# Kernel optimization log

Measured on AMD Instinct MI355X. Metric: run time of the kernel, lower is better.

The kernel has to match this reference:

```python
import jax, jax.numpy as jnp
import numpy as np

N = 100000   # nodes
R = 4        # relations
E = 200000   # edges per relation
IN = 256
HID = 64
OUT = 64
H = 8        # heads
NEG_SLOPE = 0.2


def setup_inputs() -> dict:
    key = jax.random.key(0)
    ks = jax.random.split(key, 13)
    s = 0.05
    return {
        "x": jax.random.normal(ks[0], (N, IN), jnp.float32),
        "src": jax.random.randint(ks[1], (R, E), 0, N),
        "dst": jax.random.randint(ks[2], (R, E), 0, N),
        "W0": jax.random.normal(ks[3], (R, IN, H * HID), jnp.float32) * s,
        "al0": jax.random.normal(ks[4], (R, H, HID), jnp.float32) * s,
        "ar0": jax.random.normal(ks[5], (R, H, HID), jnp.float32) * s,
        "W1": jax.random.normal(ks[6], (R, H * HID, H * HID), jnp.float32) * s,
        "al1": jax.random.normal(ks[7], (R, H, HID), jnp.float32) * s,
        "ar1": jax.random.normal(ks[8], (R, H, HID), jnp.float32) * s,
        "W2": jax.random.normal(ks[9], (R, H * HID, H * OUT), jnp.float32) * s,
        "al2": jax.random.normal(ks[10], (R, H, OUT), jnp.float32) * s,
        "ar2": jax.random.normal(ks[11], (R, H, OUT), jnp.float32) * s,
    }


def gat_layer(h, src, dst, W, al, ar):
    """Multi-relation GATConv layer; HeteroGraphConv sums ELU'd per-relation outputs.
    h: [N, in]; W: [R, in, H*O]; al/ar: [R, H, O]. Returns [N, H, O]."""
    n = h.shape[0]
    nheads, odim = al.shape[1], al.shape[2]
    acc = jnp.zeros((n, nheads, odim), h.dtype)
    for r in range(W.shape[0]):  # small fixed relation count
        f = (h @ W[r]).reshape(n, nheads, odim)          # [N,H,O]
        el = jnp.sum(f * al[r], axis=-1)                  # [N,H]
        er = jnp.sum(f * ar[r], axis=-1)                  # [N,H]
        s_r, d_r = src[r], dst[r]
        e = jax.nn.leaky_relu(el[s_r] + er[d_r], NEG_SLOPE)  # [E,H]
        # segment softmax over incoming edges per destination node
        m = jax.ops.segment_max(e, d_r, num_segments=n)
        m = jnp.where(jnp.isfinite(m), m, 0.0)
        ex = jnp.exp(e - m[d_r])
        denom = jax.ops.segment_sum(ex, d_r, num_segments=n)
        alpha = ex / (denom[d_r] + 1e-9)                  # [E,H]
        msg = f[s_r] * alpha[:, :, None]                  # [E,H,O]
        out_r = jax.ops.segment_sum(msg, d_r, num_segments=n)  # [N,H,O]
        acc = acc + jax.nn.elu(out_r)
    return acc


def reference(x, src, dst, W0, al0, ar0, W1, al1, ar1, W2, al2, ar2):
    h = gat_layer(x, src, dst, W0, al0, ar0).reshape(N, -1)   # flatten heads
    h = gat_layer(h, src, dst, W1, al1, ar1).reshape(N, -1)   # flatten heads
    h = gat_layer(h, src, dst, W2, al2, ar2).mean(axis=1)     # mean over heads
    return h
```

## Files before the change

kernel.cpp:

```cpp
#include <hip/hip_runtime.h>
#include <hip/hip_bf16.h>
#include <math.h>

#define NNODES 100000
#define NREL 4
#define NEDGE 200000
#define NH 8
#define FDIM 512
#define NMB256 391

typedef float f4 __attribute__((ext_vector_type(4)));
typedef __bf16 bf16x8 __attribute__((ext_vector_type(8)));
typedef __bf16 bf16x4 __attribute__((ext_vector_type(4)));

__device__ __forceinline__ float eluf(float v) { return v > 0.f ? v : expm1f(v); }
__device__ __forceinline__ void gload16(const __bf16* g, __bf16* l) {
  __builtin_amdgcn_global_load_lds((const __attribute__((address_space(1))) void*)g,
                                   (__attribute__((address_space(3))) void*)l, 16, 0, 0);
}

__global__ void k_conv(const float* __restrict__ in, __bf16* __restrict__ outp) {
  int i = (blockIdx.x * 256 + threadIdx.x) * 4;
  f4 v = *(const f4*)(in + i);
  bf16x4 o = {(__bf16)v.x, (__bf16)v.y, (__bf16)v.z, (__bf16)v.w};
  *(bf16x4*)(outp + i) = o;
}

__global__ void k_transW(const float* __restrict__ W, __bf16* __restrict__ Wt, int K) {
  __shared__ float tile[32][33];
  int r = blockIdx.z;
  const float* Wr = W + (size_t)r * K * FDIM;
  __bf16* Wtr = Wt + (size_t)r * FDIM * K;
  int k0 = blockIdx.x * 32, n0 = blockIdx.y * 32;
  int tx = threadIdx.x, ty = threadIdx.y;
  for (int i = ty; i < 32; i += 8)
    tile[i][tx] = Wr[(size_t)(k0 + i) * FDIM + n0 + tx];
  __syncthreads();
  for (int i = ty; i < 32; i += 8)
    Wtr[(size_t)(n0 + i) * K + k0 + tx] = (__bf16)tile[tx][i];
}

__global__ __launch_bounds__(512, 2) void k_gemm(const __bf16* __restrict__ A,
                                                 const __bf16* __restrict__ BT,
                                                 __bf16* __restrict__ C,
                                                 const float* __restrict__ al,
                                                 const float* __restrict__ ar,
                                                 __bf16* __restrict__ el,
                                                 __bf16* __restrict__ er, int M, int K) {
  __shared__ alignas(16) __bf16 lds[3][4][128 * 32];
  int t = threadIdx.x, l = t & 63, w = t >> 6;
  int nwg = gridDim.x, q8 = nwg >> 3, r8 = nwg & 7;
  int xx = blockIdx.x & 7, loc = blockIdx.x >> 3;
  int swz = (xx < r8 ? xx * (q8 + 1) : r8 * (q8 + 1) + (xx - r8) * q8) + loc;
  int m0 = (swz >> 1) * 256, n0 = (swz & 1) * 256;
  int wm = (w >> 2) * 128, wn = (w & 3) * 64;
  f4 acc[8][4] = {};

  int srow = t >> 2;
  int scol = ((t & 3) ^ (srow & 3)) * 8;
  const __bf16* pS[4];
  {
    int ra0 = m0 + srow;       if (ra0 >= M) ra0 = M - 1;
    int ra1 = m0 + 128 + srow; if (ra1 >= M) ra1 = M - 1;
    pS[0] = A + (size_t)ra0 * K + scol;
    pS[1] = A + (size_t)ra1 * K + scol;
    pS[2] = BT + (size_t)(n0 + srow) * K + scol;
    pS[3] = BT + (size_t)(n0 + 128 + srow) * K + scol;
  }
#define STG(tile, rgn) gload16(pS[rgn] + (size_t)(tile) * 32, &lds[(tile) % 3][rgn][t * 8])

  int roff = ((l >> 4) ^ (l & 3)) * 8;
  int areg = w >> 2;
  int breg = 2 + ((w & 3) >> 1);
  int brow0 = (w & 1) * 64;

  int nt = K >> 5;
#pragma unroll
  for (int g = 0; g < 4; g++) STG(0, g);
#pragma unroll
  for (int g = 0; g < 4; g++) STG(1, g);
  asm volatile("s_waitcnt vmcnt(4)" :::);
  __builtin_amdgcn_s_barrier();
  __builtin_amdgcn_sched_barrier(0);

  for (int k = 0; k < nt; k++) {
    int bk = k % 3;
    bool stg = (k + 2) < nt;
    bf16x8 b[4], af[4];
#pragma unroll
    for (int j = 0; j < 4; j++)
      b[j] = *(const bf16x8*)(&lds[bk][breg][(brow0 + j * 16 + (l & 15)) * 32 + roff]);
#pragma unroll
    for (int i = 0; i < 4; i++)
      af[i] = *(const bf16x8*)(&lds[bk][areg][(i * 16 + (l & 15)) * 32 + roff]);
    if (stg) { STG(k + 2, 0); STG(k + 2, 1); }
    __builtin_amdgcn_s_barrier();
    asm volatile("s_waitcnt lgkmcnt(0)" ::: "memory");
    __builtin_amdgcn_sched_barrier(0);
    __builtin_amdgcn_s_setprio(1);
#pragma unroll
    for (int i = 0; i < 4; i++)
#pragma unroll
      for (int j = 0; j < 4; j++)
        acc[i][j] = __builtin_amdgcn_mfma_f32_16x16x32_bf16(af[i], b[j], acc[i][j], 0, 0, 0);
    __builtin_amdgcn_s_setprio(0);
    __builtin_amdgcn_s_barrier();
    __builtin_amdgcn_sched_barrier(0);
#pragma unroll
    for (int i = 0; i < 4; i++)
      af[i] = *(const bf16x8*)(&lds[bk][areg][(64 + i * 16 + (l & 15)) * 32 + roff]);
    if (stg) { STG(k + 2, 2); STG(k + 2, 3); }
    if (k + 2 < nt)      asm volatile("s_waitcnt vmcnt(4)" :::);
    else if (k + 1 < nt) asm volatile("s_waitcnt vmcnt(0)" :::);
    __builtin_amdgcn_s_barrier();
    asm volatile("s_waitcnt lgkmcnt(0)" ::: "memory");
    __builtin_amdgcn_sched_barrier(0);
    __builtin_amdgcn_s_setprio(1);
#pragma unroll
    for (int i = 0; i < 4; i++)
#pragma unroll
      for (int j = 0; j < 4; j++)
        acc[4 + i][j] = __builtin_amdgcn_mfma_f32_16x16x32_bf16(af[i], b[j], acc[4 + i][j], 0, 0, 0);
    __builtin_amdgcn_s_setprio(0);
    __builtin_amdgcn_s_barrier();
    __builtin_amdgcn_sched_barrier(0);
  }
#undef STG

  int cn = n0 + wn + (l & 15);
  int rbase = m0 + wm + (l >> 4) * 4;
#pragma unroll
  for (int i = 0; i < 8; i++)
#pragma unroll
    for (int q2 = 0; q2 < 4; q2++) {
      int row = rbase + i * 16 + q2;
      if (row < M) {
#pragma unroll
        for (int j = 0; j < 4; j++)
          C[(size_t)row * FDIM + cn + j * 16] = (__bf16)acc[i][j][q2];
      }
    }

  int h = (n0 + wn) >> 6;
  float av[4], bv[4];
#pragma unroll
  for (int j = 0; j < 4; j++) {
    av[j] = al[h * 64 + j * 16 + (l & 15)];
    bv[j] = ar[h * 64 + j * 16 + (l & 15)];
  }
#pragma unroll
  for (int i = 0; i < 8; i++)
#pragma unroll
    for (int q2 = 0; q2 < 4; q2++) {
      float se = acc[i][0][q2] * av[0] + acc[i][1][q2] * av[1] +
                 acc[i][2][q2] * av[2] + acc[i][3][q2] * av[3];
      float sr = acc[i][0][q2] * bv[0] + acc[i][1][q2] * bv[1] +
                 acc[i][2][q2] * bv[2] + acc[i][3][q2] * bv[3];
      se += __shfl_xor(se, 1); se += __shfl_xor(se, 2);
      se += __shfl_xor(se, 4); se += __shfl_xor(se, 8);
      sr += __shfl_xor(sr, 1); sr += __shfl_xor(sr, 2);
      sr += __shfl_xor(sr, 4); sr += __shfl_xor(sr, 8);
      if ((l & 15) == 0) {
        int row = rbase + i * 16 + q2;
        if (row < M) {
          el[row * NH + h] = (__bf16)se;
          er[row * NH + h] = (__bf16)sr;
        }
      }
    }
}

__global__ void k_count(const int* __restrict__ dst, int* __restrict__ deg) {
  int e = blockIdx.x * 256 + threadIdx.x;
  int r = blockIdx.y;
  if (e < NEDGE) {
    int d = dst[(size_t)r * NEDGE + e];
    if ((unsigned)d < (unsigned)NNODES) atomicAdd(&deg[r * NNODES + d], 1);
  }
}

__global__ __launch_bounds__(256) void k_scan_a(const int* __restrict__ in, int* __restrict__ out,
                                                int* __restrict__ bsum, int n) {
  __shared__ int wsums[4];
  int t = threadIdx.x, lane = t & 63, w = t >> 6;
  int base = blockIdx.x * 1024 + t * 4;
  int v0 = base + 0 < n ? in[base + 0] : 0;
  int v1 = base + 1 < n ? in[base + 1] : 0;
  int v2 = base + 2 < n ? in[base + 2] : 0;
  int v3 = base + 3 < n ? in[base + 3] : 0;
  int tot = v0 + v1 + v2 + v3;
  int sc = tot;
#pragma unroll
  for (int off = 1; off < 64; off <<= 1) {
    int u = __shfl_up(sc, off);
    if (lane >= off) sc += u;
  }
  if (lane == 63) wsums[w] = sc;
  __syncthreads();
  int add = 0;
#pragma unroll
  for (int i = 0; i < 4; i++)
    if (i < w) add += wsums[i];
  int excl = add + sc - tot;
  if (base + 0 < n) out[base + 0] = excl;
  if (base + 1 < n) out[base + 1] = excl + v0;
  if (base + 2 < n) out[base + 2] = excl + v0 + v1;
  if (base + 3 < n) out[base + 3] = excl + v0 + v1 + v2;
  if (t == 255) bsum[blockIdx.x] = add + sc;
}

__global__ __launch_bounds__(256) void k_scan_b(int* __restrict__ bsum, int nb) {
  __shared__ int wsums[4];
  int t = threadIdx.x, lane = t & 63, w = t >> 6;
  int i0 = t * 2, i1 = t * 2 + 1;
  int v0 = i0 < nb ? bsum[i0] : 0;
  int v1 = i1 < nb ? bsum[i1] : 0;
  int tot = v0 + v1, sc = tot;
#pragma unroll
  for (int off = 1; off < 64; off <<= 1) {
    int u = __shfl_up(sc, off);
    if (lane >= off) sc += u;
  }
  if (lane == 63) wsums[w] = sc;
  __syncthreads();
  int add = 0;
#pragma unroll
  for (int i = 0; i < 4; i++)
    if (i < w) add += wsums[i];
  int excl = add + sc - tot;
  if (i0 < nb) bsum[i0] = excl;
  if (i1 < nb) bsum[i1] = excl + v0;
}

__global__ void k_scan_c(int* __restrict__ out, const int* __restrict__ bsum, int n) {
  int i = blockIdx.x * 256 + threadIdx.x;
  if (i < n) out[i] += bsum[i >> 10];
}

__global__ void k_scatter(const int* __restrict__ src, const int* __restrict__ dst,
                          const int* __restrict__ ptrf, int* __restrict__ cur,
                          int* __restrict__ csrc) {
  int e = blockIdx.x * 256 + threadIdx.x;
  int r = blockIdx.y;
  if (e >= NEDGE) return;
  int d = dst[(size_t)r * NEDGE + e];
  if ((unsigned)d >= (unsigned)NNODES) return;
  int slot = ptrf[r * NNODES + d] + atomicAdd(&cur[r * NNODES + d], 1);
  if ((unsigned)slot < (unsigned)(NREL * NEDGE))
    csrc[slot] = src[(size_t)r * NEDGE + e];
}

__global__ void k_agg(const __bf16* __restrict__ f, const __bf16* __restrict__ el,
                      const __bf16* __restrict__ er, const int* __restrict__ ptrf,
                      const int* __restrict__ deg, const int* __restrict__ csrc,
                      __bf16* __restrict__ accG, int writeMode) {
  int t = threadIdx.x;
  int l = t & 63;
  int d = blockIdx.x * 4 + (t >> 6);
  int h = l >> 3;
  int cnt = deg[d];
  float res[8] = {0.f, 0.f, 0.f, 0.f, 0.f, 0.f, 0.f, 0.f};
  if (cnt > 0) {
    int start = ptrf[d];
    if (start < 0) start = 0;
    if (start > NREL * NEDGE) start = NREL * NEDGE;
    if (cnt > NREL * NEDGE - start) cnt = NREL * NEDGE - start;
    float erh = (float)er[d * NH + h];
    float a[8] = {0.f, 0.f, 0.f, 0.f, 0.f, 0.f, 0.f, 0.f};
    float den = 0.f;
    for (int j = 0; j < cnt; j++) {
      int s = csrc[start + j];
      if ((unsigned)s >= (unsigned)NNODES) s = 0;
      float e = (float)el[s * NH + h] + erh;
      e = (e > 0.f) ? e : 0.2f * e;
      float ex = __expf(e);
      den += ex;
      bf16x8 fv = *(const bf16x8*)(f + (size_t)s * FDIM + l * 8);
#pragma unroll
      for (int i = 0; i < 8; i++) a[i] += ex * (float)fv[i];
    }
    float inv = 1.f / (den + 1e-9f);
#pragma unroll
    for (int i = 0; i < 8; i++) res[i] = eluf(a[i] * inv);
  } else if (!writeMode) {
    return;
  }
  __bf16* ap = accG + (size_t)d * FDIM + l * 8;
  bf16x8 o;
  if (writeMode) {
#pragma unroll
    for (int i = 0; i < 8; i++) o[i] = (__bf16)res[i];
  } else {
    bf16x8 cv = *(bf16x8*)ap;
#pragma unroll
    for (int i = 0; i < 8; i++) o[i] = (__bf16)((float)cv[i] + res[i]);
  }
  *(bf16x8*)ap = o;
}

__global__ void k_mean(const __bf16* __restrict__ acc, float* __restrict__ out) {
  int t = blockIdx.x * 256 + threadIdx.x;
  int n = t >> 6, o = t & 63;
  const __bf16* ap = acc + (size_t)n * FDIM + o;
  float s = 0.f;
#pragma unroll
  for (int h = 0; h < 8; h++) s += (float)ap[h * 64];
  out[t] = s * 0.125f;
}

extern "C" void kernel_launch(void* const* d_in, const int* in_sizes, int n_in,
                              void* d_out, int out_size, void* d_ws, size_t ws_size,
                              hipStream_t stream) {
  const float* x = (const float*)d_in[0];
  const int* srcp = (const int*)d_in[1];
  const int* dstp = (const int*)d_in[2];
  const float* Wl[3]  = {(const float*)d_in[3], (const float*)d_in[6], (const float*)d_in[9]};
  const float* alp[3] = {(const float*)d_in[4], (const float*)d_in[7], (const float*)d_in[10]};
  const float* arl[3] = {(const float*)d_in[5], (const float*)d_in[8], (const float*)d_in[11]};
  float* out = (float*)d_out;
  (void)in_sizes; (void)n_in; (void)out_size;

  auto rup = [](size_t b) { return (b + 255) & ~(size_t)255; };
  size_t need = 3 * rup((size_t)NNODES * FDIM * 2) +
                2 * rup((size_t)NNODES * NH * 2) +
                rup((size_t)NREL * FDIM * FDIM * 2) +
                3 * rup((size_t)NREL * NNODES * 4) +
                rup((size_t)NREL * NEDGE * 4) + rup(4096);
  if (ws_size < need) return;

  char* ws = (char*)d_ws;
  size_t off = 0;
  auto alloc = [&](size_t bytes) -> void* { void* p = ws + off; off += rup(bytes); return p; };
  __bf16* bufA = (__bf16*)alloc((size_t)NNODES * FDIM * 2);
  __bf16* bufB = (__bf16*)alloc((size_t)NNODES * FDIM * 2);
  __bf16* fbuf = (__bf16*)alloc((size_t)NNODES * FDIM * 2);
  __bf16* el   = (__bf16*)alloc((size_t)NNODES * NH * 2);
  __bf16* er   = (__bf16*)alloc((size_t)NNODES * NH * 2);
  __bf16* Wt   = (__bf16*)alloc((size_t)NREL * FDIM * FDIM * 2);
  int* deg  = (int*)alloc((size_t)NREL * NNODES * 4);
  int* ptrf = (int*)alloc((size_t)NREL * NNODES * 4);
  int* cur  = (int*)alloc((size_t)NREL * NNODES * 4);
  int* csrc = (int*)alloc((size_t)NREL * NEDGE * 4);
  int* bsum = (int*)alloc(4096);

  hipMemsetAsync(deg, 0, (size_t)NREL * NNODES * 4, stream);
  hipMemsetAsync(cur, 0, (size_t)NREL * NNODES * 4, stream);
  k_count<<<dim3((NEDGE + 255) / 256, NREL), 256, 0, stream>>>(dstp, deg);
  int ntot = NREL * NNODES;
  int nb1 = (ntot + 1023) / 1024;
  k_scan_a<<<nb1, 256, 0, stream>>>(deg, ptrf, bsum, ntot);
  k_scan_b<<<1, 256, 0, stream>>>(bsum, nb1);
  k_scan_c<<<(ntot + 255) / 256, 256, 0, stream>>>(ptrf, bsum, ntot);
  k_scatter<<<dim3((NEDGE + 255) / 256, NREL), 256, 0, stream>>>(srcp, dstp, ptrf, cur, csrc);

  k_conv<<<(NNODES * 256) / 1024, 256, 0, stream>>>(x, bufA);

  __bf16* inb = bufA;
  __bf16* outb = bufB;
  int ngrid = NMB256 * 2;
  for (int L = 0; L < 3; L++) {
    int K = (L == 0) ? 256 : FDIM;
    k_transW<<<dim3(K / 32, 16, NREL), dim3(32, 8), 0, stream>>>(Wl[L], Wt, K);
    for (int r = 0; r < NREL; r++) {
      k_gemm<<<ngrid, 512, 0, stream>>>(inb, Wt + (size_t)r * FDIM * K, fbuf,
                                        alp[L] + (size_t)r * 512,
                                        arl[L] + (size_t)r * 512,
                                        el, er, NNODES, K);
      k_agg<<<NNODES / 4, 256, 0, stream>>>(fbuf, el, er, ptrf + (size_t)r * NNODES,
                                            deg + (size_t)r * NNODES, csrc, outb,
                                            r == 0 ? 1 : 0);
    }
    __bf16* tmp = inb; inb = outb; outb = tmp;
  }
  k_mean<<<(NNODES * 64) / 256, 256, 0, stream>>>(inb, out);
}
```

Measured before the change: 2.263 ms.

## Replace LDS-pipelined GEMM with direct-load tiles; unroll aggregation; fuse final mean

The 256x256 LDS-staged, triple-buffered GEMM is replaced with a simpler 128x128 tile kernel in which each wave loads MFMA operands straight from global memory, with no LDS and no barriers. The edge aggregation loop is unrolled by two with separate accumulators to raise memory-level parallelism. The last layer's aggregation now does the head mean and writes fp32 output directly, removing the separate mean kernel and the bf16 accumulator round trip. Workspace is trimmed by aliasing the scatter scratch onto the feature buffer. The GEMM gives up LDS data reuse, which can raise global and L2 traffic.

```diff
diff --git a/kernel.cpp b/kernel.cpp
--- a/kernel.cpp
+++ b/kernel.cpp
@@ -7,17 +7,13 @@
 #define NEDGE 200000
 #define NH 8
 #define FDIM 512
-#define NMB256 391
+#define NMB 782
 
 typedef float f4 __attribute__((ext_vector_type(4)));
 typedef __bf16 bf16x8 __attribute__((ext_vector_type(8)));
 typedef __bf16 bf16x4 __attribute__((ext_vector_type(4)));
 
 __device__ __forceinline__ float eluf(float v) { return v > 0.f ? v : expm1f(v); }
-__device__ __forceinline__ void gload16(const __bf16* g, __bf16* l) {
-  __builtin_amdgcn_global_load_lds((const __attribute__((address_space(1))) void*)g,
-                                   (__attribute__((address_space(3))) void*)l, 16, 0, 0);
-}
 
 __global__ void k_conv(const float* __restrict__ in, __bf16* __restrict__ outp) {
   int i = (blockIdx.x * 256 + threadIdx.x) * 4;
@@ -40,97 +36,50 @@
     Wtr[(size_t)(n0 + i) * K + k0 + tx] = (__bf16)tile[tx][i];
 }
 
-__global__ __launch_bounds__(512, 2) void k_gemm(const __bf16* __restrict__ A,
-                                                 const __bf16* __restrict__ BT,
-                                                 __bf16* __restrict__ C,
-                                                 const float* __restrict__ al,
-                                                 const float* __restrict__ ar,
-                                                 __bf16* __restrict__ el,
-                                                 __bf16* __restrict__ er, int M, int K) {
-  __shared__ alignas(16) __bf16 lds[3][4][128 * 32];
+__global__ __launch_bounds__(256) void k_gemm(const __bf16* __restrict__ A,
+                                              const __bf16* __restrict__ BT,
+                                              __bf16* __restrict__ C,
+                                              const float* __restrict__ al,
+                                              const float* __restrict__ ar,
+                                              __bf16* __restrict__ el,
+                                              __bf16* __restrict__ er, int M, int K) {
   int t = threadIdx.x, l = t & 63, w = t >> 6;
   int nwg = gridDim.x, q8 = nwg >> 3, r8 = nwg & 7;
   int xx = blockIdx.x & 7, loc = blockIdx.x >> 3;
   int swz = (xx < r8 ? xx * (q8 + 1) : r8 * (q8 + 1) + (xx - r8) * q8) + loc;
-  int m0 = (swz >> 1) * 256, n0 = (swz & 1) * 256;
-  int wm = (w >> 2) * 128, wn = (w & 3) * 64;
-  f4 acc[8][4] = {};
-
-  int srow = t >> 2;
-  int scol = ((t & 3) ^ (srow & 3)) * 8;
-  const __bf16* pS[4];
-  {
-    int ra0 = m0 + srow;       if (ra0 >= M) ra0 = M - 1;
-    int ra1 = m0 + 128 + srow; if (ra1 >= M) ra1 = M - 1;
-    pS[0] = A + (size_t)ra0 * K + scol;
-    pS[1] = A + (size_t)ra1 * K + scol;
-    pS[2] = BT + (size_t)(n0 + srow) * K + scol;
-    pS[3] = BT + (size_t)(n0 + 128 + srow) * K + scol;
-  }
-#define STG(tile, rgn) gload16(pS[rgn] + (size_t)(tile) * 32, &lds[(tile) % 3][rgn][t * 8])
-
-  int roff = ((l >> 4) ^ (l & 3)) * 8;
-  int areg = w >> 2;
-  int breg = 2 + ((w & 3) >> 1);
-  int brow0 = (w & 1) * 64;
+  int m0 = (swz >> 2) * 128, n0 = (swz & 3) * 128;
+  int wm = (w >> 1) * 64, wn = (w & 1) * 64;
+  f4 acc[4][4] = {};
+
+  const __bf16* pa[4];
+  const __bf16* pb[4];
+#pragma unroll
+  for (int i = 0; i < 4; i++) {
+    int row = m0 + wm + i * 16 + (l & 15);
+    if (row >= M) row = M - 1;
+    pa[i] = A + (size_t)row * K + (l >> 4) * 8;
+    pb[i] = BT + (size_t)(n0 + wn + i * 16 + (l & 15)) * K + (l >> 4) * 8;
+  }
 
   int nt = K >> 5;
-#pragma unroll
-  for (int g = 0; g < 4; g++) STG(0, g);
-#pragma unroll
-  for (int g = 0; g < 4; g++) STG(1, g);
-  asm volatile("s_waitcnt vmcnt(4)" :::);
-  __builtin_amdgcn_s_barrier();
-  __builtin_amdgcn_sched_barrier(0);
-
-  for (int k = 0; k < nt; k++) {
-    int bk = k % 3;
-    bool stg = (k + 2) < nt;
-    bf16x8 b[4], af[4];
-#pragma unroll
-    for (int j = 0; j < 4; j++)
-      b[j] = *(const bf16x8*)(&lds[bk][breg][(brow0 + j * 16 + (l & 15)) * 32 + roff]);
+#pragma unroll 2
+  for (int kt = 0; kt < nt; kt++) {
+    bf16x8 a[4], b[4];
+#pragma unroll
+    for (int i = 0; i < 4; i++) a[i] = *(const bf16x8*)(pa[i] + kt * 32);
+#pragma unroll
+    for (int j = 0; j < 4; j++) b[j] = *(const bf16x8*)(pb[j] + kt * 32);
 #pragma unroll
     for (int i = 0; i < 4; i++)
-      af[i] = *(const bf16x8*)(&lds[bk][areg][(i * 16 + (l & 15)) * 32 + roff]);
-    if (stg) { STG(k + 2, 0); STG(k + 2, 1); }
-    __builtin_amdgcn_s_barrier();
-    asm volatile("s_waitcnt lgkmcnt(0)" ::: "memory");
-    __builtin_amdgcn_sched_barrier(0);
-    __builtin_amdgcn_s_setprio(1);
-#pragma unroll
-    for (int i = 0; i < 4; i++)
 #pragma unroll
       for (int j = 0; j < 4; j++)
-        acc[i][j] = __builtin_amdgcn_mfma_f32_16x16x32_bf16(af[i], b[j], acc[i][j], 0, 0, 0);
-    __builtin_amdgcn_s_setprio(0);
-    __builtin_amdgcn_s_barrier();
-    __builtin_amdgcn_sched_barrier(0);
-#pragma unroll
-    for (int i = 0; i < 4; i++)
-      af[i] = *(const bf16x8*)(&lds[bk][areg][(64 + i * 16 + (l & 15)) * 32 + roff]);
-    if (stg) { STG(k + 2, 2); STG(k + 2, 3); }
-    if (k + 2 < nt)      asm volatile("s_waitcnt vmcnt(4)" :::);
-    else if (k + 1 < nt) asm volatile("s_waitcnt vmcnt(0)" :::);
-    __builtin_amdgcn_s_barrier();
-    asm volatile("s_waitcnt lgkmcnt(0)" ::: "memory");
-    __builtin_amdgcn_sched_barrier(0);
-    __builtin_amdgcn_s_setprio(1);
-#pragma unroll
-    for (int i = 0; i < 4; i++)
-#pragma unroll
-      for (int j = 0; j < 4; j++)
-        acc[4 + i][j] = __builtin_amdgcn_mfma_f32_16x16x32_bf16(af[i], b[j], acc[4 + i][j], 0, 0, 0);
-    __builtin_amdgcn_s_setprio(0);
-    __builtin_amdgcn_s_barrier();
-    __builtin_amdgcn_sched_barrier(0);
-  }
-#undef STG
+        acc[i][j] = __builtin_amdgcn_mfma_f32_16x16x32_bf16(a[i], b[j], acc[i][j], 0, 0, 0);
+  }
 
   int cn = n0 + wn + (l & 15);
   int rbase = m0 + wm + (l >> 4) * 4;
 #pragma unroll
-  for (int i = 0; i < 8; i++)
+  for (int i = 0; i < 4; i++)
 #pragma unroll
     for (int q2 = 0; q2 < 4; q2++) {
       int row = rbase + i * 16 + q2;
@@ -149,7 +98,7 @@
     bv[j] = ar[h * 64 + j * 16 + (l & 15)];
   }
 #pragma unroll
-  for (int i = 0; i < 8; i++)
+  for (int i = 0; i < 4; i++)
 #pragma unroll
     for (int q2 = 0; q2 < 4; q2++) {
       float se = acc[i][0][q2] * av[0] + acc[i][1][q2] * av[1] +
@@ -266,22 +215,42 @@
     if (start > NREL * NEDGE) start = NREL * NEDGE;
     if (cnt > NREL * NEDGE - start) cnt = NREL * NEDGE - start;
     float erh = (float)er[d * NH + h];
-    float a[8] = {0.f, 0.f, 0.f, 0.f, 0.f, 0.f, 0.f, 0.f};
+    float a0[8] = {0.f, 0.f, 0.f, 0.f, 0.f, 0.f, 0.f, 0.f};
+    float a1[8] = {0.f, 0.f, 0.f, 0.f, 0.f, 0.f, 0.f, 0.f};
     float den = 0.f;
-    for (int j = 0; j < cnt; j++) {
-      int s = csrc[start + j];
-      if ((unsigned)s >= (unsigned)NNODES) s = 0;
-      float e = (float)el[s * NH + h] + erh;
-      e = (e > 0.f) ? e : 0.2f * e;
-      float ex = __expf(e);
-      den += ex;
-      bf16x8 fv = *(const bf16x8*)(f + (size_t)s * FDIM + l * 8);
-#pragma unroll
-      for (int i = 0; i < 8; i++) a[i] += ex * (float)fv[i];
+    int j = 0;
+    for (; j + 1 < cnt; j += 2) {
+      int s0 = csrc[start + j], s1 = csrc[start + j + 1];
+      if ((unsigned)s0 >= (unsigned)NNODES) s0 = 0;
+      if ((unsigned)s1 >= (unsigned)NNODES) s1 = 0;
+      bf16x8 fv0 = *(const bf16x8*)(f + (size_t)s0 * FDIM + l * 8);
+      bf16x8 fv1 = *(const bf16x8*)(f + (size_t)s1 * FDIM + l * 8);
+      float e0 = (float)el[s0 * NH + h] + erh;
+      float e1 = (float)el[s1 * NH + h] + erh;
+      e0 = (e0 > 0.f) ? e0 : 0.2f * e0;
+      e1 = (e1 > 0.f) ? e1 : 0.2f * e1;
+      float ex0 = __expf(e0), ex1 = __expf(e1);
+      den += ex0 + ex1;
+#pragma unroll
+      for (int i = 0; i < 8; i++) {
+        a0[i] += ex0 * (float)fv0[i];
+        a1[i] += ex1 * (float)fv1[i];
+      }
+    }
+    if (j < cnt) {
+      int s0 = csrc[start + j];
+      if ((unsigned)s0 >= (unsigned)NNODES) s0 = 0;
+      bf16x8 fv0 = *(const bf16x8*)(f + (size_t)s0 * FDIM + l * 8);
+      float e0 = (float)el[s0 * NH + h] + erh;
+      e0 = (e0 > 0.f) ? e0 : 0.2f * e0;
+      float ex0 = __expf(e0);
+      den += ex0;
+#pragma unroll
+      for (int i = 0; i < 8; i++) a0[i] += ex0 * (float)fv0[i];
     }
     float inv = 1.f / (den + 1e-9f);
 #pragma unroll
-    for (int i = 0; i < 8; i++) res[i] = eluf(a[i] * inv);
+    for (int i = 0; i < 8; i++) res[i] = eluf((a0[i] + a1[i]) * inv);
   } else if (!writeMode) {
     return;
   }
@@ -298,14 +267,77 @@
   *(bf16x8*)ap = o;
 }
 
-__global__ void k_mean(const __bf16* __restrict__ acc, float* __restrict__ out) {
-  int t = blockIdx.x * 256 + threadIdx.x;
-  int n = t >> 6, o = t & 63;
-  const __bf16* ap = acc + (size_t)n * FDIM + o;
-  float s = 0.f;
-#pragma unroll
-  for (int h = 0; h < 8; h++) s += (float)ap[h * 64];
-  out[t] = s * 0.125f;
+__global__ void k_aggm(const __bf16* __restrict__ f, const __bf16* __restrict__ el,
+                       const __bf16* __restrict__ er, const int* __restrict__ ptrf,
+                       const int* __restrict__ deg, const int* __restrict__ csrc,
+                       float* __restrict__ out, int writeMode) {
+  int t = threadIdx.x;
+  int l = t & 63;
+  int d = blockIdx.x * 4 + (t >> 6);
+  int h = l >> 3;
+  int cnt = deg[d];
+  float res[8] = {0.f, 0.f, 0.f, 0.f, 0.f, 0.f, 0.f, 0.f};
+  if (cnt > 0) {
+    int start = ptrf[d];
+    if (start < 0) start = 0;
+    if (start > NREL * NEDGE) start = NREL * NEDGE;
+    if (cnt > NREL * NEDGE - start) cnt = NREL * NEDGE - start;
+    float erh = (float)er[d * NH + h];
+    float a0[8] = {0.f, 0.f, 0.f, 0.f, 0.f, 0.f, 0.f, 0.f};
+    float a1[8] = {0.f, 0.f, 0.f, 0.f, 0.f, 0.f, 0.f, 0.f};
+    float den = 0.f;
+    int j = 0;
+    for (; j + 1 < cnt; j += 2) {
+      int s0 = csrc[start + j], s1 = csrc[start + j + 1];
+      if ((unsigned)s0 >= (unsigned)NNODES) s0 = 0;
+      if ((unsigned)s1 >= (unsigned)NNODES) s1 = 0;
+      bf16x8 fv0 = *(const bf16x8*)(f + (size_t)s0 * FDIM + l * 8);
+      bf16x8 fv1 = *(const bf16x8*)(f + (size_t)s1 * FDIM + l * 8);
+      float e0 = (float)el[s0 * NH + h] + erh;
+      float e1 = (float)el[s1 * NH + h] + erh;
+      e0 = (e0 > 0.f) ? e0 : 0.2f * e0;
+      e1 = (e1 > 0.f) ? e1 : 0.2f * e1;
+      float ex0 = __expf(e0), ex1 = __expf(e1);
+      den += ex0 + ex1;
+#pragma unroll
+      for (int i = 0; i < 8; i++) {
+        a0[i] += ex0 * (float)fv0[i];
+        a1[i] += ex1 * (float)fv1[i];
+      }
+    }
+    if (j < cnt) {
+      int s0 = csrc[start + j];
+      if ((unsigned)s0 >= (unsigned)NNODES) s0 = 0;
+      bf16x8 fv0 = *(const bf16x8*)(f + (size_t)s0 * FDIM + l * 8);
+      float e0 = (float)el[s0 * NH + h] + erh;
+      e0 = (e0 > 0.f) ? e0 : 0.2f * e0;
+      float ex0 = __expf(e0);
+      den += ex0;
+#pragma unroll
+      for (int i = 0; i < 8; i++) a0[i] += ex0 * (float)fv0[i];
+    }
+    float inv = 1.f / (den + 1e-9f);
+#pragma unroll
+    for (int i = 0; i < 8; i++) res[i] = eluf((a0[i] + a1[i]) * inv);
+  }
+#pragma unroll
+  for (int i = 0; i < 8; i++) {
+    res[i] += __shfl_xor(res[i], 8);
+    res[i] += __shfl_xor(res[i], 16);
+    res[i] += __shfl_xor(res[i], 32);
+  }
+  if (l < 8) {
+    float* op = out + (size_t)d * 64 + l * 8;
+    f4 v0 = {res[0] * 0.125f, res[1] * 0.125f, res[2] * 0.125f, res[3] * 0.125f};
+    f4 v1 = {res[4] * 0.125f, res[5] * 0.125f, res[6] * 0.125f, res[7] * 0.125f};
+    if (writeMode) {
+      ((f4*)op)[0] = v0;
+      ((f4*)op)[1] = v1;
+    } else {
+      ((f4*)op)[0] += v0;
+      ((f4*)op)[1] += v1;
+    }
+  }
 }
 
 extern "C" void kernel_launch(void* const* d_in, const int* in_sizes, int n_in,
@@ -324,24 +356,24 @@
   size_t need = 3 * rup((size_t)NNODES * FDIM * 2) +
                 2 * rup((size_t)NNODES * NH * 2) +
                 rup((size_t)NREL * FDIM * FDIM * 2) +
-                3 * rup((size_t)NREL * NNODES * 4) +
-                rup((size_t)NREL * NEDGE * 4) + rup(4096);
+                2 * rup((size_t)NREL * NNODES * 4) +
+                rup((size_t)NREL * NEDGE * 4);
   if (ws_size < need) return;
 
   char* ws = (char*)d_ws;
   size_t off = 0;
   auto alloc = [&](size_t bytes) -> void* { void* p = ws + off; off += rup(bytes); return p; };
-  __bf16* bufA = (__bf16*)alloc((size_t)NNODES * FDIM * 2);
-  __bf16* bufB = (__bf16*)alloc((size_t)NNODES * FDIM * 2);
+  __bf16* b0   = (__bf16*)alloc((size_t)NNODES * FDIM * 2);
+  __bf16* b1   = (__bf16*)alloc((size_t)NNODES * FDIM * 2);
   __bf16* fbuf = (__bf16*)alloc((size_t)NNODES * FDIM * 2);
   __bf16* el   = (__bf16*)alloc((size_t)NNODES * NH * 2);
   __bf16* er   = (__bf16*)alloc((size_t)NNODES * NH * 2);
   __bf16* Wt   = (__bf16*)alloc((size_t)NREL * FDIM * FDIM * 2);
   int* deg  = (int*)alloc((size_t)NREL * NNODES * 4);
   int* ptrf = (int*)alloc((size_t)NREL * NNODES * 4);
-  int* cur  = (int*)alloc((size_t)NREL * NNODES * 4);
   int* csrc = (int*)alloc((size_t)NREL * NEDGE * 4);
-  int* bsum = (int*)alloc(4096);
+  int* cur  = (int*)fbuf;
+  int* bsum = (int*)((char*)fbuf + rup((size_t)NREL * NNODES * 4));
 
   hipMemsetAsync(deg, 0, (size_t)NREL * NNODES * 4, stream);
   hipMemsetAsync(cur, 0, (size_t)NREL * NNODES * 4, stream);
@@ -353,24 +385,27 @@
   k_scan_c<<<(ntot + 255) / 256, 256, 0, stream>>>(ptrf, bsum, ntot);
   k_scatter<<<dim3((NEDGE + 255) / 256, NREL), 256, 0, stream>>>(srcp, dstp, ptrf, cur, csrc);
 
-  k_conv<<<(NNODES * 256) / 1024, 256, 0, stream>>>(x, bufA);
-
-  __bf16* inb = bufA;
-  __bf16* outb = bufB;
-  int ngrid = NMB256 * 2;
+  k_conv<<<(NNODES * 256) / 1024, 256, 0, stream>>>(x, b1);
+
+  int ngrid = NMB * 4;
   for (int L = 0; L < 3; L++) {
     int K = (L == 0) ? 256 : FDIM;
+    const __bf16* inb = (L == 1) ? b0 : b1;
+    __bf16* outb = (L == 0) ? b0 : b1;
     k_transW<<<dim3(K / 32, 16, NREL), dim3(32, 8), 0, stream>>>(Wl[L], Wt, K);
     for (int r = 0; r < NREL; r++) {
-      k_gemm<<<ngrid, 512, 0, stream>>>(inb, Wt + (size_t)r * FDIM * K, fbuf,
+      k_gemm<<<ngrid, 256, 0, stream>>>(inb, Wt + (size_t)r * FDIM * K, fbuf,
                                         alp[L] + (size_t)r * 512,
                                         arl[L] + (size_t)r * 512,
                                         el, er, NNODES, K);
-      k_agg<<<NNODES / 4, 256, 0, stream>>>(fbuf, el, er, ptrf + (size_t)r * NNODES,
-                                            deg + (size_t)r * NNODES, csrc, outb,
-                                            r == 0 ? 1 : 0);
-    }
-    __bf16* tmp = inb; inb = outb; outb = tmp;
-  }
-  k_mean<<<(NNODES * 64) / 256, 256, 0, stream>>>(inb, out);
-}
+      if (L < 2)
+        k_agg<<<NNODES / 4, 256, 0, stream>>>(fbuf, el, er, ptrf + (size_t)r * NNODES,
+                                              deg + (size_t)r * NNODES, csrc, outb,
+                                              r == 0 ? 1 : 0);
+      else
+        k_aggm<<<NNODES / 4, 256, 0, stream>>>(fbuf, el, er, ptrf + (size_t)r * NNODES,
+                                               deg + (size_t)r * NNODES, csrc, out,
+                                               r == 0 ? 1 : 0);
+    }
+  }
+}
```

Measured after the change: 2.922 ms. 1.29x slower.
